# Kernel optimization log

Hardware: AMD Instinct MI355X
Metric: run time of the kernel (lower is better)

Reference implementation:

```python
import jax, jax.numpy as jnp
import numpy as np

ATTN = 128

def _gelu(x):
    return jax.nn.gelu(x, approximate=False)

def _mlp3(x, W1, b1, W2, b2, W3, b3):
    h = _gelu(x @ W1.T + b1)
    h = _gelu(h @ W2.T + b2)
    return h @ W3.T + b3

def setup_inputs() -> dict:
    key = jax.random.key(0)
    ks = jax.random.split(key, 32)
    B, K, M, C = 128, 64, 2048, 32
    QD, AD, H = 128, 128, 256
    s = 0.02
    d = {}
    d['g'] = jax.random.normal(ks[0], (B, K, 3), dtype=jnp.float32)
    d['query'] = jax.random.normal(ks[1], (M, QD), dtype=jnp.float32) * s
    d['qW'] = jax.random.normal(ks[2], (AD, QD), dtype=jnp.float32) * s
    d['qb'] = jnp.zeros((AD,), jnp.float32)
    d['kW'] = jax.random.normal(ks[3], (AD, 1), dtype=jnp.float32) * s
    d['kb'] = jnp.zeros((AD,), jnp.float32)
    # global_mlp: K -> H -> H -> H
    d['gm_W1'] = jax.random.normal(ks[4], (H, K), dtype=jnp.float32) * s
    d['gm_b1'] = jnp.zeros((H,), jnp.float32)
    d['gm_W2'] = jax.random.normal(ks[5], (H, H), dtype=jnp.float32) * s
    d['gm_b2'] = jnp.zeros((H,), jnp.float32)
    d['gm_W3'] = jax.random.normal(ks[6], (H, H), dtype=jnp.float32) * s
    d['gm_b3'] = jnp.zeros((H,), jnp.float32)
    # point_mlp: (H+QD+1) -> H -> H -> H
    d['pm_W1'] = jax.random.normal(ks[7], (H, H + QD + 1), dtype=jnp.float32) * s
    d['pm_b1'] = jnp.zeros((H,), jnp.float32)
    d['pm_W2'] = jax.random.normal(ks[8], (H, H), dtype=jnp.float32) * s
    d['pm_b2'] = jnp.zeros((H,), jnp.float32)
    d['pm_W3'] = jax.random.normal(ks[9], (H, H), dtype=jnp.float32) * s
    d['pm_b3'] = jnp.zeros((H,), jnp.float32)
    d['tW'] = jax.random.normal(ks[10], (C, H), dtype=jnp.float32) * s
    d['tb'] = jnp.zeros((C,), jnp.float32)
    d['wW'] = jax.random.normal(ks[11], (1, H), dtype=jnp.float32) * s
    d['wb'] = jnp.zeros((1,), jnp.float32)
    d['cW'] = jax.random.normal(ks[12], (1, H), dtype=jnp.float32) * s
    d['cb'] = jnp.zeros((1,), jnp.float32)
    return d

def reference(g, query, qW, qb, kW, kb,
              gm_W1, gm_b1, gm_W2, gm_b2, gm_W3, gm_b3,
              pm_W1, pm_b1, pm_W2, pm_b2, pm_W3, pm_b3,
              tW, tb, wW, wb, cW, cb):
    B, K, _ = g.shape
    M = query.shape[0]
    inv = jnp.linalg.norm(g, axis=-1)                    # (B,K)
    Q = query @ qW.T + qb                                # (M,AD)
    Kk = inv[..., None] * kW[:, 0] + kb                  # (B,K,AD) Linear(1->AD)
    scores = jnp.einsum('md,bkd->bmk', Q, Kk) / jnp.sqrt(jnp.float32(Q.shape[-1]))
    A = jax.nn.softmax(scores, axis=-1)                  # (B,M,K)
    y = jnp.einsum('bmk,bkd->bmd', A, g)                 # (B,M,3)
    global_s = _mlp3(inv, gm_W1, gm_b1, gm_W2, gm_b2, gm_W3, gm_b3)  # (B,H)
    attended_inv = jnp.einsum('bmk,bk->bm', A, inv)      # (B,M)
    s_in = jnp.concatenate([
        jnp.broadcast_to(global_s[:, None, :], (B, M, global_s.shape[-1])),
        jnp.broadcast_to(query[None], (B, M, query.shape[-1])),
        attended_inv[..., None],
    ], axis=-1)                                          # (B,M,H+QD+1)
    s = _mlp3(s_in, pm_W1, pm_b1, pm_W2, pm_b2, pm_W3, pm_b3)  # (B,M,H)
    type_logits = s @ tW.T + tb                          # (B,M,C)
    weight_logits = (s @ wW.T + wb)[..., 0]              # (B,M)
    gate = jnp.clip(jax.nn.sigmoid(s @ cW.T + cb), 0.0, 1.0)  # (B,M,1)
    y = y * gate
    return (y, type_logits, weight_logits)
```

## Files before the change

kernel.cpp:

```cpp
#include <hip/hip_runtime.h>
#include <math.h>


typedef __attribute__((ext_vector_type(8))) short short8;
typedef __attribute__((ext_vector_type(4))) float f32x4;

__device__ __forceinline__ unsigned short bf16_rne(float f){
    union { float f; unsigned u; } v; v.f = f;
    return (unsigned short)((v.u + 0x7FFFu + ((v.u >> 16) & 1u)) >> 16);
}

__device__ __forceinline__ float gelu_f(float x){
    float z  = x * 0.70710678118654752f;
    float az = fabsf(z);
    float t  = __builtin_amdgcn_rcpf(1.0f + 0.3275911f * az);
    float p  = t*(0.254829592f + t*(-0.284496736f + t*(1.421413741f + t*(-1.453152027f + t*1.061405429f))));
    float e  = __expf(-az*az);
    float er = copysignf(1.0f - p*e, z);
    return 0.5f * x * (1.0f + er);
}

__global__ void k_pre1(const float* __restrict__ g, const float* __restrict__ qW,
                       const float* __restrict__ qb, const float* __restrict__ kW,
                       const float* __restrict__ query, const float* __restrict__ pmW1,
                       const float* __restrict__ pmW2, const float* __restrict__ pmW3,
                       const float* __restrict__ pmb3,
                       const float* __restrict__ tW, const float* __restrict__ tb,
                       const float* __restrict__ wW, const float* __restrict__ wb,
                       const float* __restrict__ cW, const float* __restrict__ cb,
                       float* __restrict__ invg, float* __restrict__ vg, float* __restrict__ s0g,
                       unsigned short* __restrict__ w2b, unsigned short* __restrict__ wheadb,
                       float* __restrict__ bheadg, float* __restrict__ u2g) {
    const int bid = blockIdx.x, tid = threadIdx.x;
    if (bid < 32) {
        int idx = bid*256 + tid;
        const float* p = g + idx*3;
        invg[idx] = sqrtf(p[0]*p[0] + p[1]*p[1] + p[2]*p[2]);
    } else if (bid == 32) {
        if (tid < 128) {
            float acc = 0.f;
            for (int d = 0; d < 128; ++d) acc += qW[d*128 + tid] * kW[d];
            vg[tid] = acc;
            if (tid == 0) {
                float s = 0.f;
                for (int d = 0; d < 128; ++d) s += qb[d] * kW[d];
                *s0g = s;
            }
        }
    } else if (bid < 97) {
        int o = (bid - 33)*1024 + tid*4;
        float4 x = *(const float4*)&pmW2[o];
        union { unsigned short u[4]; uint2 v; } r;
        r.u[0] = bf16_rne(x.x); r.u[1] = bf16_rne(x.y);
        r.u[2] = bf16_rne(x.z); r.u[3] = bf16_rne(x.w);
        *(uint2*)&w2b[o] = r.v;
    } else if (bid < 131) {
        __shared__ float hw[256];
        int c = bid - 97;
        const float* src = (c < 32) ? (tW + c*256) : ((c == 32) ? wW : cW);
        hw[tid] = src[tid];
        __syncthreads();
        float acc = 0.f;
        for (int j = 0; j < 256; ++j) acc += hw[j] * pmW3[j*256 + tid];
        wheadb[c*256 + tid] = bf16_rne(acc);
        if (tid == 0) {
            float bacc = (c < 32) ? tb[c] : ((c == 32) ? wb[0] : cb[0]);
            for (int j = 0; j < 256; ++j) bacc += hw[j] * pmb3[j];
            bheadg[c] = bacc;
        }
    } else {
        __shared__ float qv[4][128];
        int mbase = (bid - 131)*4;
        if (tid < 128) {
            #pragma unroll
            for (int mm = 0; mm < 4; ++mm) qv[mm][tid] = query[(mbase+mm)*128 + tid];
        }
        __syncthreads();
        const float* wp = pmW1 + tid*385 + 256;
        float a0=0.f, a1=0.f, a2=0.f, a3=0.f;
        for (int e = 0; e < 128; ++e) {
            float wv = wp[e];
            a0 += wv*qv[0][e]; a1 += wv*qv[1][e];
            a2 += wv*qv[2][e]; a3 += wv*qv[3][e];
        }
        u2g[(mbase+0)*256 + tid] = a0;
        u2g[(mbase+1)*256 + tid] = a1;
        u2g[(mbase+2)*256 + tid] = a2;
        u2g[(mbase+3)*256 + tid] = a3;
    }
}

__global__ void k_pre2(const float* __restrict__ query, const float* __restrict__ vg,
                       const float* __restrict__ s0g, const float* __restrict__ invg,
                       const float* __restrict__ gmW1, const float* __restrict__ gmb1,
                       const float* __restrict__ gmW2, const float* __restrict__ gmb2,
                       const float* __restrict__ gmW3, const float* __restrict__ gmb3,
                       const float* __restrict__ pmW1, const float* __restrict__ pmb1,
                       float* __restrict__ ag, float* __restrict__ u1g) {
    const int bid = blockIdx.x, tid = threadIdx.x;
    if (bid < 8) {
        __shared__ float vs[128];
        if (tid < 128) vs[tid] = vg[tid];
        __syncthreads();
        int m = bid*256 + tid;
        const float4* qp = (const float4*)(query + m*128);
        float acc = *s0g;
        #pragma unroll 8
        for (int e4 = 0; e4 < 32; ++e4) {
            float4 q = qp[e4];
            acc += q.x*vs[e4*4] + q.y*vs[e4*4+1] + q.z*vs[e4*4+2] + q.w*vs[e4*4+3];
        }
        ag[m] = acc * 0.08838834764831845f;
    } else {
        __shared__ float s_in[64];
        __shared__ float s_h[256];
        __shared__ float s_h2[256];
        int b = bid - 8;
        if (tid < 64) s_in[tid] = invg[b*64 + tid];
        __syncthreads();
        float acc = gmb1[tid];
        #pragma unroll 4
        for (int k = 0; k < 64; k += 4) {
            float4 w = *(const float4*)&gmW1[tid*64 + k];
            acc += w.x*s_in[k] + w.y*s_in[k+1] + w.z*s_in[k+2] + w.w*s_in[k+3];
        }
        s_h[tid] = gelu_f(acc);
        __syncthreads();
        acc = gmb2[tid];
        #pragma unroll 4
        for (int i = 0; i < 256; i += 4) {
            float4 w = *(const float4*)&gmW2[tid*256 + i];
            acc += w.x*s_h[i] + w.y*s_h[i+1] + w.z*s_h[i+2] + w.w*s_h[i+3];
        }
        s_h2[tid] = gelu_f(acc);
        __syncthreads();
        acc = gmb3[tid];
        #pragma unroll 4
        for (int i = 0; i < 256; i += 4) {
            float4 w = *(const float4*)&gmW3[tid*256 + i];
            acc += w.x*s_h2[i] + w.y*s_h2[i+1] + w.z*s_h2[i+2] + w.w*s_h2[i+3];
        }
        __syncthreads();
        s_h[tid] = acc;
        __syncthreads();
        float u = pmb1[tid];
        const float* w1 = pmW1 + tid*385;
        for (int i = 0; i < 256; ++i) u += w1[i] * s_h[i];
        u1g[b*256 + tid] = u;
    }
}

__global__ __launch_bounds__(256, 4)
void k_main(const float* __restrict__ g,
            const float* __restrict__ invg, const float* __restrict__ ag,
            const float* __restrict__ u1g, const float* __restrict__ u2g,
            const float* __restrict__ pmW1, const float* __restrict__ pmb2,
            const unsigned short* __restrict__ w2b, const unsigned short* __restrict__ wheadb,
            const float* __restrict__ bheadg, float* __restrict__ out) {
    __shared__ __align__(16) unsigned short hb[64*264];
    __shared__ float invs[64], gsl[192], u1s[256], w385s[256], pmb2s[256];
    __shared__ float ainv_s[64], y0s[192];

    const int tid = threadIdx.x;
    const int bid = blockIdx.x;
    const int b  = bid >> 5;
    const int m0 = (bid & 31) << 6;

    if (tid < 64)  invs[tid] = invg[b*64 + tid];
    if (tid < 192) gsl[tid]  = g[b*192 + tid];
    u1s[tid]   = u1g[b*256 + tid];
    w385s[tid] = pmW1[tid*385 + 384];
    pmb2s[tid] = pmb2[tid];
    __syncthreads();

    {
        const int r = tid >> 2, sub = tid & 3;
        const float am = ag[m0 + r];
        const int kb = sub * 16;
        float mx = -1e30f;
        #pragma unroll
        for (int i = 0; i < 16; ++i) mx = fmaxf(mx, invs[kb + i] * am);
        #pragma unroll
        for (int d = 1; d < 4; d <<= 1) mx = fmaxf(mx, __shfl_xor(mx, d, 64));
        float den = 0.f, ai = 0.f, y0 = 0.f, y1 = 0.f, y2 = 0.f;
        #pragma unroll
        for (int i = 0; i < 16; ++i) {
            const int k = kb + i;
            const float iv = invs[k];
            const float e = __expf(iv * am - mx);
            den += e; ai += e * iv;
            y0 += e * gsl[k*3+0]; y1 += e * gsl[k*3+1]; y2 += e * gsl[k*3+2];
        }
        #pragma unroll
        for (int d = 1; d < 4; d <<= 1) {
            den += __shfl_xor(den, d, 64);
            ai  += __shfl_xor(ai , d, 64);
            y0  += __shfl_xor(y0 , d, 64);
            y1  += __shfl_xor(y1 , d, 64);
            y2  += __shfl_xor(y2 , d, 64);
        }
        if (sub == 0) {
            const float id = 1.0f / den;
            ainv_s[r] = ai * id;
            y0s[r*3+0] = y0*id; y0s[r*3+1] = y1*id; y0s[r*3+2] = y2*id;
        }
    }
    __syncthreads();

    const int w = tid >> 6, lane = tid & 63;

    {
        const int r = lane, j0 = w * 64;
        const float aiv = ainv_s[r];
        const float4* u2p = (const float4*)(u2g + (size_t)(m0 + r)*256 + j0);
        #pragma unroll
        for (int c8 = 0; c8 < 8; ++c8) {
            float4 ua = u2p[c8*2];
            float4 ub = u2p[c8*2 + 1];
            float xs[8] = {ua.x, ua.y, ua.z, ua.w, ub.x, ub.y, ub.z, ub.w};
            short8 vh;
            #pragma unroll
            for (int i = 0; i < 8; ++i) {
                const int j = j0 + c8*8 + i;
                const float x = u1s[j] + xs[i] + aiv * w385s[j];
                vh[i] = (short)bf16_rne(gelu_f(x));
            }
            *(short8*)&hb[r*264 + j0 + c8*8] = vh;
        }
    }
    __syncthreads();

    const int q = lane >> 4, ln = lane & 15;
    f32x4 acc[4][4];
    #pragma unroll
    for (int mt = 0; mt < 4; ++mt)
        #pragma unroll
        for (int nt = 0; nt < 4; ++nt) acc[mt][nt] = (f32x4){0.f,0.f,0.f,0.f};

    #pragma unroll 2
    for (int kk = 0; kk < 8; ++kk) {
        const int kc = kk*32 + q*8;
        short8 afrag[4], bfrag[4];
        #pragma unroll
        for (int mt = 0; mt < 4; ++mt)
            afrag[mt] = *(const short8*)&hb[(mt*16 + ln)*264 + kc];
        #pragma unroll
        for (int nt = 0; nt < 4; ++nt)
            bfrag[nt] = *(const short8*)&w2b[(w*64 + nt*16 + ln)*256 + kc];
        #pragma unroll
        for (int mt = 0; mt < 4; ++mt)
            #pragma unroll
            for (int nt = 0; nt < 4; ++nt)
                acc[mt][nt] = __builtin_amdgcn_mfma_f32_16x16x32_bf16(afrag[mt], bfrag[nt], acc[mt][nt], 0, 0, 0);
    }
    __syncthreads();

    #pragma unroll
    for (int mt = 0; mt < 4; ++mt) {
        #pragma unroll
        for (int nt = 0; nt < 4; ++nt) {
            const int n = w*64 + nt*16 + ln;
            const float bb = pmb2s[n];
            #pragma unroll
            for (int rg = 0; rg < 4; ++rg) {
                const int r = mt*16 + q*4 + rg;
                hb[r*264 + n] = bf16_rne(gelu_f(acc[mt][nt][rg] + bb));
            }
        }
    }
    __syncthreads();

    f32x4 accA0 = {0.f,0.f,0.f,0.f}, accA1 = {0.f,0.f,0.f,0.f}, accB = {0.f,0.f,0.f,0.f};
    const int rr = w*16 + ln;
    const int cb2 = (ln < 2) ? (32 + ln) : 33;
    #pragma unroll 2
    for (int kk = 0; kk < 8; ++kk) {
        const int kc = kk*32 + q*8;
        short8 bh = *(const short8*)&hb[rr*264 + kc];
        short8 a0 = *(const short8*)&wheadb[ ln      *256 + kc];
        short8 a1 = *(const short8*)&wheadb[(16 + ln)*256 + kc];
        short8 a2 = *(const short8*)&wheadb[ cb2     *256 + kc];
        accA0 = __builtin_amdgcn_mfma_f32_16x16x32_bf16(a0, bh, accA0, 0, 0, 0);
        accA1 = __builtin_amdgcn_mfma_f32_16x16x32_bf16(a1, bh, accA1, 0, 0, 0);
        accB  = __builtin_amdgcn_mfma_f32_16x16x32_bf16(a2, bh, accB , 0, 0, 0);
    }
    {
        const size_t row = (size_t)b*2048 + m0 + rr;
        const int c0 = q*4;
        f32x4 r0 = accA0 + *(const f32x4*)&bheadg[c0];
        f32x4 r1 = accA1 + *(const f32x4*)&bheadg[16 + c0];
        *(f32x4*)&out[786432 + row*32 + c0]      = r0;
        *(f32x4*)&out[786432 + row*32 + 16 + c0] = r1;
        if (q == 0) {
            out[9175040 + row] = accB[0] + bheadg[32];
            float gv = accB[1] + bheadg[33];
            float gt = 1.0f / (1.0f + __expf(-gv));
            gt = fminf(fmaxf(gt, 0.0f), 1.0f);
            float* yo = out + row*3;
            yo[0] = y0s[rr*3+0] * gt;
            yo[1] = y0s[rr*3+1] * gt;
            yo[2] = y0s[rr*3+2] * gt;
        }
    }
}

extern "C" void kernel_launch(void* const* d_in, const int* in_sizes, int n_in,
                              void* d_out, int out_size, void* d_ws, size_t ws_size,
                              hipStream_t stream) {
    const float* g     = (const float*)d_in[0];
    const float* query = (const float*)d_in[1];
    const float* qW    = (const float*)d_in[2];
    const float* qb    = (const float*)d_in[3];
    const float* kW    = (const float*)d_in[4];
    const float* gmW1  = (const float*)d_in[6];
    const float* gmb1  = (const float*)d_in[7];
    const float* gmW2  = (const float*)d_in[8];
    const float* gmb2  = (const float*)d_in[9];
    const float* gmW3  = (const float*)d_in[10];
    const float* gmb3  = (const float*)d_in[11];
    const float* pmW1  = (const float*)d_in[12];
    const float* pmb1  = (const float*)d_in[13];
    const float* pmW2  = (const float*)d_in[14];
    const float* pmb2  = (const float*)d_in[15];
    const float* pmW3  = (const float*)d_in[16];
    const float* pmb3  = (const float*)d_in[17];
    const float* tW    = (const float*)d_in[18];
    const float* tb    = (const float*)d_in[19];
    const float* wW    = (const float*)d_in[20];
    const float* wb    = (const float*)d_in[21];
    const float* cW    = (const float*)d_in[22];
    const float* cb    = (const float*)d_in[23];
    float* out = (float*)d_out;

    float* ws    = (float*)d_ws;
    float* invg  = ws;
    float* ag    = ws + 8192;
    float* vg    = ws + 10240;
    float* s0g   = ws + 10368;
    float* u1g   = ws + 10496;
    float* u2g   = ws + 43264;
    unsigned short* w2b    = (unsigned short*)(ws + 567552);
    unsigned short* wheadb = (unsigned short*)(ws + 600320);
    float* bheadg = ws + 604672;

    hipLaunchKernelGGL(k_pre1, dim3(643), dim3(256), 0, stream,
                       g, qW, qb, kW, query, pmW1, pmW2, pmW3, pmb3,
                       tW, tb, wW, wb, cW, cb,
                       invg, vg, s0g, w2b, wheadb, bheadg, u2g);
    hipLaunchKernelGGL(k_pre2, dim3(136), dim3(256), 0, stream,
                       query, vg, s0g, invg,
                       gmW1, gmb1, gmW2, gmb2, gmW3, gmb3, pmW1, pmb1,
                       ag, u1g);
    hipLaunchKernelGGL(k_main, dim3(4096), dim3(256), 0, stream,
                       g, invg, ag, u1g, u2g, pmW1, pmb2,
                       w2b, wheadb, bheadg, out);
}
```

Measured before the change: 288.7 us.

## Compute query-projection in main kernel via MFMA and use sigmoid-form fast GELU

Drops the precomputed fp32 query projection buffer (u2g, 2048x256). Each main block now computes its query x W1q slice with bf16 MFMA from bf16 copies of query and W1q, which removes a large global read per block and the scalar precompute. GELU in the main kernel is replaced by a sigmoid-based exp2 approximation, and the global-MLP weights are pre-transposed so k_pre2 reads them coalesced. This adds MFMA work, lowers precision through bf16 inputs and the approximate GELU, and grows the prep kernel with transpose blocks.

```diff
diff --git a/kernel.cpp b/kernel.cpp
--- a/kernel.cpp
+++ b/kernel.cpp
@@ -20,17 +20,32 @@
     return 0.5f * x * (1.0f + er);
 }
 
+__device__ __forceinline__ float gelu_fast(float x){
+    float x2 = x*x;
+    float p  = fmaf(x2, -0.1029433f, -2.3022082f);
+    float u  = x*p;
+    float e  = __builtin_amdgcn_exp2f(u);
+    float r  = __builtin_amdgcn_rcpf(1.0f + e);
+    return x*r;
+}
+
 __global__ void k_pre1(const float* __restrict__ g, const float* __restrict__ qW,
                        const float* __restrict__ qb, const float* __restrict__ kW,
                        const float* __restrict__ query, const float* __restrict__ pmW1,
                        const float* __restrict__ pmW2, const float* __restrict__ pmW3,
                        const float* __restrict__ pmb3,
+                       const float* __restrict__ gmW1, const float* __restrict__ gmW2,
+                       const float* __restrict__ gmW3,
                        const float* __restrict__ tW, const float* __restrict__ tb,
                        const float* __restrict__ wW, const float* __restrict__ wb,
                        const float* __restrict__ cW, const float* __restrict__ cb,
                        float* __restrict__ invg, float* __restrict__ vg, float* __restrict__ s0g,
                        unsigned short* __restrict__ w2b, unsigned short* __restrict__ wheadb,
-                       float* __restrict__ bheadg, float* __restrict__ u2g) {
+                       float* __restrict__ bheadg,
+                       unsigned short* __restrict__ w1qb, unsigned short* __restrict__ queryb,
+                       float* __restrict__ gmW1t, float* __restrict__ gmW2t,
+                       float* __restrict__ gmW3t, float* __restrict__ w1gt,
+                       float* __restrict__ w385g) {
     const int bid = blockIdx.x, tid = threadIdx.x;
     if (bid < 32) {
         int idx = bid*256 + tid;
@@ -68,34 +83,55 @@
             for (int j = 0; j < 256; ++j) bacc += hw[j] * pmb3[j];
             bheadg[c] = bacc;
         }
+    } else if (bid < 163) {
+        int o = (bid - 131)*1024 + tid*4;
+        int n = o >> 7, k = o & 127;
+        union { unsigned short u[4]; uint2 v; } r;
+        #pragma unroll
+        for (int i = 0; i < 4; ++i) r.u[i] = bf16_rne(pmW1[n*385 + 256 + k + i]);
+        *(uint2*)&w1qb[o] = r.v;
+    } else if (bid < 227) {
+        int base = (bid - 163)*4096 + tid*4;
+        #pragma unroll
+        for (int it = 0; it < 4; ++it) {
+            int o = base + it*1024;
+            float4 x = *(const float4*)&query[o];
+            union { unsigned short u[4]; uint2 v; } r;
+            r.u[0] = bf16_rne(x.x); r.u[1] = bf16_rne(x.y);
+            r.u[2] = bf16_rne(x.z); r.u[3] = bf16_rne(x.w);
+            *(uint2*)&queryb[o] = r.v;
+        }
+    } else if (bid < 291) {
+        int o = (bid - 227)*1024 + tid*4;
+        int i = o >> 8, j = o & 255;
+        float4 r = { gmW2[j*256+i], gmW2[(j+1)*256+i], gmW2[(j+2)*256+i], gmW2[(j+3)*256+i] };
+        *(float4*)&gmW2t[o] = r;
+    } else if (bid < 355) {
+        int o = (bid - 291)*1024 + tid*4;
+        int i = o >> 8, j = o & 255;
+        float4 r = { gmW3[j*256+i], gmW3[(j+1)*256+i], gmW3[(j+2)*256+i], gmW3[(j+3)*256+i] };
+        *(float4*)&gmW3t[o] = r;
+    } else if (bid < 419) {
+        int o = (bid - 355)*1024 + tid*4;
+        int i = o >> 8, j = o & 255;
+        float4 r = { pmW1[j*385+i], pmW1[(j+1)*385+i], pmW1[(j+2)*385+i], pmW1[(j+3)*385+i] };
+        *(float4*)&w1gt[o] = r;
+    } else if (bid < 435) {
+        int o = (bid - 419)*1024 + tid*4;
+        int k = o >> 8, j = o & 255;
+        float4 r = { gmW1[j*64+k], gmW1[(j+1)*64+k], gmW1[(j+2)*64+k], gmW1[(j+3)*64+k] };
+        *(float4*)&gmW1t[o] = r;
     } else {
-        __shared__ float qv[4][128];
-        int mbase = (bid - 131)*4;
-        if (tid < 128) {
-            #pragma unroll
-            for (int mm = 0; mm < 4; ++mm) qv[mm][tid] = query[(mbase+mm)*128 + tid];
-        }
-        __syncthreads();
-        const float* wp = pmW1 + tid*385 + 256;
-        float a0=0.f, a1=0.f, a2=0.f, a3=0.f;
-        for (int e = 0; e < 128; ++e) {
-            float wv = wp[e];
-            a0 += wv*qv[0][e]; a1 += wv*qv[1][e];
-            a2 += wv*qv[2][e]; a3 += wv*qv[3][e];
-        }
-        u2g[(mbase+0)*256 + tid] = a0;
-        u2g[(mbase+1)*256 + tid] = a1;
-        u2g[(mbase+2)*256 + tid] = a2;
-        u2g[(mbase+3)*256 + tid] = a3;
+        w385g[tid] = pmW1[tid*385 + 384];
     }
 }
 
 __global__ void k_pre2(const float* __restrict__ query, const float* __restrict__ vg,
                        const float* __restrict__ s0g, const float* __restrict__ invg,
-                       const float* __restrict__ gmW1, const float* __restrict__ gmb1,
-                       const float* __restrict__ gmW2, const float* __restrict__ gmb2,
-                       const float* __restrict__ gmW3, const float* __restrict__ gmb3,
-                       const float* __restrict__ pmW1, const float* __restrict__ pmb1,
+                       const float* __restrict__ gmW1t, const float* __restrict__ gmb1,
+                       const float* __restrict__ gmW2t, const float* __restrict__ gmb2,
+                       const float* __restrict__ gmW3t, const float* __restrict__ gmb3,
+                       const float* __restrict__ w1gt, const float* __restrict__ pmb1,
                        float* __restrict__ ag, float* __restrict__ u1g) {
     const int bid = blockIdx.x, tid = threadIdx.x;
     if (bid < 8) {
@@ -119,33 +155,24 @@
         if (tid < 64) s_in[tid] = invg[b*64 + tid];
         __syncthreads();
         float acc = gmb1[tid];
-        #pragma unroll 4
-        for (int k = 0; k < 64; k += 4) {
-            float4 w = *(const float4*)&gmW1[tid*64 + k];
-            acc += w.x*s_in[k] + w.y*s_in[k+1] + w.z*s_in[k+2] + w.w*s_in[k+3];
-        }
+        #pragma unroll 8
+        for (int k = 0; k < 64; ++k) acc += gmW1t[k*256 + tid] * s_in[k];
         s_h[tid] = gelu_f(acc);
         __syncthreads();
         acc = gmb2[tid];
-        #pragma unroll 4
-        for (int i = 0; i < 256; i += 4) {
-            float4 w = *(const float4*)&gmW2[tid*256 + i];
-            acc += w.x*s_h[i] + w.y*s_h[i+1] + w.z*s_h[i+2] + w.w*s_h[i+3];
-        }
+        #pragma unroll 8
+        for (int i = 0; i < 256; ++i) acc += gmW2t[i*256 + tid] * s_h[i];
         s_h2[tid] = gelu_f(acc);
         __syncthreads();
         acc = gmb3[tid];
-        #pragma unroll 4
-        for (int i = 0; i < 256; i += 4) {
-            float4 w = *(const float4*)&gmW3[tid*256 + i];
-            acc += w.x*s_h2[i] + w.y*s_h2[i+1] + w.z*s_h2[i+2] + w.w*s_h2[i+3];
-        }
+        #pragma unroll 8
+        for (int i = 0; i < 256; ++i) acc += gmW3t[i*256 + tid] * s_h2[i];
         __syncthreads();
         s_h[tid] = acc;
         __syncthreads();
         float u = pmb1[tid];
-        const float* w1 = pmW1 + tid*385;
-        for (int i = 0; i < 256; ++i) u += w1[i] * s_h[i];
+        #pragma unroll 8
+        for (int i = 0; i < 256; ++i) u += w1gt[i*256 + tid] * s_h[i];
         u1g[b*256 + tid] = u;
     }
 }
@@ -153,8 +180,9 @@
 __global__ __launch_bounds__(256, 4)
 void k_main(const float* __restrict__ g,
             const float* __restrict__ invg, const float* __restrict__ ag,
-            const float* __restrict__ u1g, const float* __restrict__ u2g,
-            const float* __restrict__ pmW1, const float* __restrict__ pmb2,
+            const float* __restrict__ u1g, const float* __restrict__ w385g,
+            const float* __restrict__ pmb2,
+            const unsigned short* __restrict__ queryb, const unsigned short* __restrict__ w1qb,
             const unsigned short* __restrict__ w2b, const unsigned short* __restrict__ wheadb,
             const float* __restrict__ bheadg, float* __restrict__ out) {
     __shared__ __align__(16) unsigned short hb[64*264];
@@ -169,7 +197,7 @@
     if (tid < 64)  invs[tid] = invg[b*64 + tid];
     if (tid < 192) gsl[tid]  = g[b*192 + tid];
     u1s[tid]   = u1g[b*256 + tid];
-    w385s[tid] = pmW1[tid*385 + 384];
+    w385s[tid] = w385g[tid];
     pmb2s[tid] = pmb2[tid];
     __syncthreads();
 
@@ -208,29 +236,47 @@
     __syncthreads();
 
     const int w = tid >> 6, lane = tid & 63;
+    const int q = lane >> 4, ln = lane & 15;
 
     {
-        const int r = lane, j0 = w * 64;
-        const float aiv = ainv_s[r];
-        const float4* u2p = (const float4*)(u2g + (size_t)(m0 + r)*256 + j0);
-        #pragma unroll
-        for (int c8 = 0; c8 < 8; ++c8) {
-            float4 ua = u2p[c8*2];
-            float4 ub = u2p[c8*2 + 1];
-            float xs[8] = {ua.x, ua.y, ua.z, ua.w, ub.x, ub.y, ub.z, ub.w};
-            short8 vh;
-            #pragma unroll
-            for (int i = 0; i < 8; ++i) {
-                const int j = j0 + c8*8 + i;
-                const float x = u1s[j] + xs[i] + aiv * w385s[j];
-                vh[i] = (short)bf16_rne(gelu_f(x));
+        f32x4 acc[4][4];
+        #pragma unroll
+        for (int mt = 0; mt < 4; ++mt)
+            #pragma unroll
+            for (int nt = 0; nt < 4; ++nt) acc[mt][nt] = (f32x4){0.f,0.f,0.f,0.f};
+        #pragma unroll
+        for (int kk = 0; kk < 4; ++kk) {
+            const int kc = kk*32 + q*8;
+            short8 afr[4], bfr[4];
+            #pragma unroll
+            for (int mt = 0; mt < 4; ++mt)
+                afr[mt] = *(const short8*)&queryb[(m0 + mt*16 + ln)*128 + kc];
+            #pragma unroll
+            for (int nt = 0; nt < 4; ++nt)
+                bfr[nt] = *(const short8*)&w1qb[(w*64 + nt*16 + ln)*128 + kc];
+            #pragma unroll
+            for (int mt = 0; mt < 4; ++mt)
+                #pragma unroll
+                for (int nt = 0; nt < 4; ++nt)
+                    acc[mt][nt] = __builtin_amdgcn_mfma_f32_16x16x32_bf16(afr[mt], bfr[nt], acc[mt][nt], 0, 0, 0);
+        }
+        #pragma unroll
+        for (int mt = 0; mt < 4; ++mt) {
+            #pragma unroll
+            for (int nt = 0; nt < 4; ++nt) {
+                const int n = w*64 + nt*16 + ln;
+                const float u1v = u1s[n], wv = w385s[n];
+                #pragma unroll
+                for (int rg = 0; rg < 4; ++rg) {
+                    const int r = mt*16 + q*4 + rg;
+                    const float x = acc[mt][nt][rg] + u1v + ainv_s[r]*wv;
+                    hb[r*264 + n] = bf16_rne(gelu_fast(x));
+                }
             }
-            *(short8*)&hb[r*264 + j0 + c8*8] = vh;
         }
     }
     __syncthreads();
 
-    const int q = lane >> 4, ln = lane & 15;
     f32x4 acc[4][4];
     #pragma unroll
     for (int mt = 0; mt < 4; ++mt)
@@ -264,7 +310,7 @@
             #pragma unroll
             for (int rg = 0; rg < 4; ++rg) {
                 const int r = mt*16 + q*4 + rg;
-                hb[r*264 + n] = bf16_rne(gelu_f(acc[mt][nt][rg] + bb));
+                hb[r*264 + n] = bf16_rne(gelu_fast(acc[mt][nt][rg] + bb));
             }
         }
     }
@@ -338,20 +384,28 @@
     float* vg    = ws + 10240;
     float* s0g   = ws + 10368;
     float* u1g   = ws + 10496;
-    float* u2g   = ws + 43264;
-    unsigned short* w2b    = (unsigned short*)(ws + 567552);
-    unsigned short* wheadb = (unsigned short*)(ws + 600320);
-    float* bheadg = ws + 604672;
-
-    hipLaunchKernelGGL(k_pre1, dim3(643), dim3(256), 0, stream,
+    float* gmW1t = ws + 43264;
+    float* gmW2t = ws + 59648;
+    float* gmW3t = ws + 125184;
+    float* w1gt  = ws + 190720;
+    float* w385g = ws + 256256;
+    float* bheadg= ws + 256512;
+    unsigned short* w2b    = (unsigned short*)(ws + 256576);
+    unsigned short* wheadb = (unsigned short*)(ws + 289344);
+    unsigned short* w1qb   = (unsigned short*)(ws + 293696);
+    unsigned short* queryb = (unsigned short*)(ws + 310080);
+
+    hipLaunchKernelGGL(k_pre1, dim3(436), dim3(256), 0, stream,
                        g, qW, qb, kW, query, pmW1, pmW2, pmW3, pmb3,
+                       gmW1, gmW2, gmW3,
                        tW, tb, wW, wb, cW, cb,
-                       invg, vg, s0g, w2b, wheadb, bheadg, u2g);
+                       invg, vg, s0g, w2b, wheadb, bheadg,
+                       w1qb, queryb, gmW1t, gmW2t, gmW3t, w1gt, w385g);
     hipLaunchKernelGGL(k_pre2, dim3(136), dim3(256), 0, stream,
                        query, vg, s0g, invg,
-                       gmW1, gmb1, gmW2, gmb2, gmW3, gmb3, pmW1, pmb1,
+                       gmW1t, gmb1, gmW2t, gmb2, gmW3t, gmb3, w1gt, pmb1,
                        ag, u1g);
     hipLaunchKernelGGL(k_main, dim3(4096), dim3(256), 0, stream,
-                       g, invg, ag, u1g, u2g, pmW1, pmb2,
-                       w2b, wheadb, bheadg, out);
-}
+                       g, invg, ag, u1g, w385g, pmb2,
+                       queryb, w1qb, w2b, wheadb, bheadg, out);
+}
```

Result: slower. 316.2 us (+9.5%).
